# Performance work log

Measured on AMD Instinct MI355X. Metric: run time of the kernel, lower is better.

Reference implementation:

```python
import jax, jax.numpy as jnp
import numpy as np

B, S_SRC, S_TGT = 32, 128, 128
V, E, H = 32000, 256, 256
PAD_ID = 0
NEG = -1.0e9


def setup_inputs() -> dict:
    key = jax.random.key(0)
    ks = jax.random.split(key, 16)
    lengths_de = jax.random.randint(ks[0], (B,), S_SRC // 2, S_SRC + 1)
    idx_de = jax.random.randint(ks[1], (B, S_SRC), 1, V)
    pos = jnp.arange(S_SRC)[None, :]
    indices_de = jnp.where(pos < lengths_de[:, None], idx_de, PAD_ID)
    indices_en = jax.random.randint(ks[2], (B, S_TGT), 1, V)
    lengths_en = jnp.full((B,), S_TGT, dtype=jnp.int32)

    sc = 0.02
    def nrm(k, shape):
        return jax.random.normal(k, shape, dtype=jnp.float32) * sc
    emb_enc = nrm(ks[3], (V, E)).at[PAD_ID].set(0.0)
    emb_dec = nrm(ks[4], (V, E)).at[PAD_ID].set(0.0)
    return {
        "indices_de": indices_de, "lengths_de": lengths_de,
        "indices_en": indices_en, "lengths_en": lengths_en,
        "emb_enc": emb_enc, "emb_dec": emb_dec,
        "W_ih_enc": nrm(ks[5], (H, E)), "W_hh_enc": nrm(ks[6], (H, H)),
        "b_ih_enc": jnp.zeros((H,), jnp.float32), "b_hh_enc": jnp.zeros((H,), jnp.float32),
        "W_ih_dec": nrm(ks[7], (H, E)), "W_hh_dec": nrm(ks[8], (H, H)),
        "b_ih_dec": jnp.zeros((H,), jnp.float32), "b_hh_dec": jnp.zeros((H,), jnp.float32),
        "W_attn": nrm(ks[9], (H, 2 * H)), "b_attn": jnp.zeros((H,), jnp.float32),
        "W_out": nrm(ks[10], (V, H)), "b_out": jnp.zeros((V,), jnp.float32),
    }


def reference(indices_de, lengths_de, indices_en, lengths_en,
              emb_enc, emb_dec,
              W_ih_enc, W_hh_enc, b_ih_enc, b_hh_enc,
              W_ih_dec, W_hh_dec, b_ih_dec, b_hh_dec,
              W_attn, b_attn, W_out, b_out):
    # ---- Encoder: tanh RNN over packed sequence ----
    x_enc = emb_enc[indices_de]                      # [B, S, E]
    valid = jnp.arange(S_SRC)[None, :] < lengths_de[:, None]  # [B, S]

    def enc_step(h, inp):
        x_t, v_t = inp                                # [B,E], [B]
        h_new = jnp.tanh(x_t @ W_ih_enc.T + b_ih_enc + h @ W_hh_enc.T + b_hh_enc)
        h = jnp.where(v_t[:, None], h_new, h)         # frozen past length (pack semantics)
        out = jnp.where(v_t[:, None], h_new, 0.0)     # padded outputs are zero
        return h, out

    h0 = jnp.zeros((B, H), jnp.float32)
    h_final, enc_outs = jax.lax.scan(
        enc_step, h0, (x_enc.transpose(1, 0, 2), valid.T))
    encoder_outputs = enc_outs.transpose(1, 0, 2)     # [B, S, H]
    enc_mask = indices_de == PAD_ID                   # [B, S] True at padding

    # ---- Decoder: per-step RNN cell + dot-product attention + vocab proj ----
    x_dec = emb_dec[indices_en]                       # [B, T, E]

    def dec_step(h, x_t):
        h = jnp.tanh(x_t @ W_ih_dec.T + b_ih_dec + h @ W_hh_dec.T + b_hh_dec)
        scores = jnp.einsum('bh,bsh->bs', h, encoder_outputs)
        scores = jnp.where(enc_mask, NEG, scores)
        attn = jax.nn.softmax(scores, axis=-1)
        context = jnp.einsum('bs,bsh->bh', attn, encoder_outputs)
        combined = jnp.concatenate([context, h], axis=1)          # [B, 2H]
        attn_out = jnp.tanh(combined @ W_attn.T + b_attn)         # [B, H]
        logits_t = attn_out @ W_out.T + b_out                     # [B, V]
        return h, logits_t

    _, logits = jax.lax.scan(dec_step, h_final, x_dec.transpose(1, 0, 2))
    return logits.transpose(1, 0, 2)                  # [B, T, V]
```

## Files before the change

### kernel.cpp

```cpp
#include <hip/hip_runtime.h>
#include <stdint.h>

#define B_ 32
#define S_ 128
#define T_ 128
#define V_ 32000
#define E_ 256
#define H_ 256
#define NEG_ (-1.0e9f)

typedef __attribute__((ext_vector_type(8))) short short8;
typedef __attribute__((ext_vector_type(4))) float floatx4;

__device__ __forceinline__ unsigned short f2bf(float x){
  unsigned u = __float_as_uint(x);
  u = u + 0x7fffu + ((u >> 16) & 1u);
  return (unsigned short)(u >> 16);
}
__device__ __forceinline__ float bf2f(unsigned short s){
  return __uint_as_float(((unsigned)s) << 16);
}
__device__ __forceinline__ float hsum4(float4 v){ return (v.x+v.y)+(v.z+v.w); }
__device__ __forceinline__ void unpack8(uint4 q, float4& lo, float4& hi){
  lo.x = __uint_as_float(q.x << 16); lo.y = __uint_as_float(q.x & 0xffff0000u);
  lo.z = __uint_as_float(q.y << 16); lo.w = __uint_as_float(q.y & 0xffff0000u);
  hi.x = __uint_as_float(q.z << 16); hi.y = __uint_as_float(q.z & 0xffff0000u);
  hi.z = __uint_as_float(q.w << 16); hi.w = __uint_as_float(q.w & 0xffff0000u);
}

#define GLOAD_LDS16(gptr, lptr) \
  __builtin_amdgcn_global_load_lds( \
      (const __attribute__((address_space(1))) unsigned int*)(const void*)(gptr), \
      (__attribute__((address_space(3))) unsigned int*)(void*)(lptr), 16, 0, 0)

#define LDS_BARRIER() do { \
    asm volatile("s_waitcnt lgkmcnt(0)" ::: "memory"); \
    __builtin_amdgcn_s_barrier(); \
  } while(0)

__device__ __forceinline__ void cvt_body(const float* __restrict__ src,
                                         unsigned short* __restrict__ dst,
                                         int blk, int n4){
  int i = blk*256 + (int)threadIdx.x;
  if (i < n4){
    float4 v = ((const float4*)src)[i];
    ushort4 o; o.x=f2bf(v.x); o.y=f2bf(v.y); o.z=f2bf(v.z); o.w=f2bf(v.w);
    ((ushort4*)dst)[i] = o;
  }
}

__device__ __forceinline__ void xih_body(
    const int* __restrict__ idxmat, const float* __restrict__ emb,
    const float* __restrict__ Wih,
    const float* __restrict__ b1, const float* __restrict__ b2,
    float* __restrict__ out, int blk,
    int* idx_s, float4 (*x_s)[64])
{
  int b = blk >> 3;
  int t0 = (blk & 7) << 4;
  int tid = threadIdx.x;
  if (tid < 16) idx_s[tid] = idxmat[b*128 + t0 + tid];
  __syncthreads();
  for (int r = 0; r < 16; ++r)
    ((float*)&x_s[r][0])[tid] = emb[(size_t)idx_s[r]*E_ + tid];
  __syncthreads();
  int j2 = tid & 127, tg = tid >> 7;
  const float4* W0 = (const float4*)(Wih + (size_t)j2*E_);
  const float4* W1 = (const float4*)(Wih + (size_t)(j2+128)*E_);
  float4 a0[8], a1[8];
  #pragma unroll
  for (int t=0;t<8;++t){ a0[t]={0,0,0,0}; a1[t]={0,0,0,0}; }
  for (int e4 = 0; e4 < 64; ++e4){
    float4 w0 = W0[e4], w1 = W1[e4];
    #pragma unroll
    for (int t = 0; t < 8; ++t){
      float4 xv = x_s[tg*8+t][e4];
      a0[t] += w0*xv; a1[t] += w1*xv;
    }
  }
  float bi0 = b1[j2] + b2[j2];
  float bi1 = b1[j2+128] + b2[j2+128];
  #pragma unroll
  for (int t = 0; t < 8; ++t){
    size_t row = (size_t)((b<<7) + t0 + tg*8 + t)*H_;
    out[row + j2]     = hsum4(a0[t]) + bi0;
    out[row + j2+128] = hsum4(a1[t]) + bi1;
  }
}

__global__ __launch_bounds__(256) void k_prep(
    const float* __restrict__ W_out, unsigned short* __restrict__ Wout_bf,
    const float* __restrict__ W_attn, unsigned short* __restrict__ Wattn_bf,
    const int* __restrict__ indices_de, const float* __restrict__ emb_enc,
    const float* __restrict__ W_ih_enc, const float* __restrict__ b_ih_enc,
    const float* __restrict__ b_hh_enc, float* __restrict__ Xih_enc,
    const int* __restrict__ indices_en, const float* __restrict__ emb_dec,
    const float* __restrict__ W_ih_dec, const float* __restrict__ b_ih_dec,
    const float* __restrict__ b_hh_dec, float* __restrict__ Xih_dec)
{
  __shared__ int idx_s[16];
  __shared__ float4 x_s[16][64];
  int bx = blockIdx.x;
  if (bx < 8000){
    cvt_body(W_out, Wout_bf, bx, 2048000);
  } else if (bx < 8128){
    cvt_body(W_attn, Wattn_bf, bx - 8000, 32768);
  } else if (bx < 8384){
    xih_body(indices_de, emb_enc, W_ih_enc, b_ih_enc, b_hh_enc, Xih_enc,
             bx - 8128, idx_s, x_s);
  } else {
    xih_body(indices_en, emb_dec, W_ih_dec, b_ih_dec, b_hh_dec, Xih_dec,
             bx - 8384, idx_s, x_s);
  }
}

__global__ __launch_bounds__(512, 2) void k_rnn2(
    const float* __restrict__ Whh_e, const float* __restrict__ Whh_d,
    const float* __restrict__ Xih_e, const float* __restrict__ Xih_d,
    const int* __restrict__ lengths,
    unsigned short* __restrict__ enc_out,
    float* __restrict__ hseq)
{
  __shared__ float h_s[256];
  __shared__ float part[8][256];
  int b = blockIdx.x, tid = threadIdx.x;
  int kk = tid >> 6;
  int jg = tid & 63;
  float4 w[4][8];
  #pragma unroll
  for (int r = 0; r < 4; ++r){
    const float4* Wr = (const float4*)(Whh_e + (size_t)(jg + (r<<6))*H_ + (kk<<5));
    #pragma unroll
    for (int i = 0; i < 8; ++i) w[r][i] = Wr[i];
  }
  if (tid < 256) h_s[tid] = 0.f;
  int len = lengths[b];
  __syncthreads();

  for (int t = 0; t < 128; ++t){
    float x = 0.f;
    if (tid < 256) x = Xih_e[(size_t)((b<<7) + t)*H_ + tid];
    const float4* h4 = ((const float4*)h_s) + (kk << 3);
    float4 hv[8];
    #pragma unroll
    for (int i = 0; i < 8; ++i) hv[i] = h4[i];
    #pragma unroll
    for (int r = 0; r < 4; ++r){
      float4 a = {0,0,0,0};
      #pragma unroll
      for (int i = 0; i < 8; ++i) a += w[r][i]*hv[i];
      part[kk][jg + (r<<6)] = hsum4(a);
    }
    LDS_BARRIER();
    if (tid < 256){
      float s = x;
      #pragma unroll
      for (int q = 0; q < 8; ++q) s += part[q][tid];
      float hn = tanhf(s);
      float hold = h_s[tid];
      bool v = (t < len);
      h_s[tid] = v ? hn : hold;
      enc_out[(size_t)((b<<7)+t)*H_ + tid] = f2bf(v ? hn : 0.f);
    }
    LDS_BARRIER();
  }

  #pragma unroll
  for (int r = 0; r < 4; ++r){
    const float4* Wr = (const float4*)(Whh_d + (size_t)(jg + (r<<6))*H_ + (kk<<5));
    #pragma unroll
    for (int i = 0; i < 8; ++i) w[r][i] = Wr[i];
  }
  for (int t = 0; t < 128; ++t){
    float x = 0.f;
    if (tid < 256) x = Xih_d[(size_t)((b<<7) + t)*H_ + tid];
    const float4* h4 = ((const float4*)h_s) + (kk << 3);
    float4 hv[8];
    #pragma unroll
    for (int i = 0; i < 8; ++i) hv[i] = h4[i];
    #pragma unroll
    for (int r = 0; r < 4; ++r){
      float4 a = {0,0,0,0};
      #pragma unroll
      for (int i = 0; i < 8; ++i) a += w[r][i]*hv[i];
      part[kk][jg + (r<<6)] = hsum4(a);
    }
    LDS_BARRIER();
    if (tid < 256){
      float s = x;
      #pragma unroll
      for (int q = 0; q < 8; ++q) s += part[q][tid];
      float hn = tanhf(s);
      h_s[tid] = hn;
      hseq[(size_t)((b<<7)+t)*H_ + tid] = hn;
    }
    LDS_BARRIER();
  }
}

__global__ __launch_bounds__(256) void k_attn(
    const unsigned short* __restrict__ enc_out,
    const float* __restrict__ hseq,
    const int* __restrict__ lengths,
    const unsigned short* __restrict__ Wattn,
    const float* __restrict__ battn,
    unsigned short* __restrict__ attn_out)
{
  __shared__ float h_sm[16][256];
  __shared__ float sc[16][132];
  __shared__ float comb[16][512];
  int bx = blockIdx.x; int b = bx >> 3; int t0 = (bx & 7) << 4;
  int tid = threadIdx.x;
  int len = lengths[b];
  for (int r = 0; r < 16; ++r)
    h_sm[r][tid] = hseq[(size_t)((b<<7) + t0 + r)*H_ + tid];
  __syncthreads();
  {
    int s = tid & 127, tg = tid >> 7;
    float4 a[8];
    #pragma unroll
    for (int t=0;t<8;++t) a[t] = {0,0,0,0};
    const uint4* ep = (const uint4*)(enc_out + (size_t)(b*S_ + s)*H_);
    for (int oct = 0; oct < 32; ++oct){
      uint4 q = ep[oct];
      float4 elo, ehi; unpack8(q, elo, ehi);
      #pragma unroll
      for (int t = 0; t < 8; ++t){
        const float4* hp = (const float4*)&h_sm[tg*8+t][oct*8];
        a[t] += elo*hp[0] + ehi*hp[1];
      }
    }
    #pragma unroll
    for (int t = 0; t < 8; ++t)
      sc[tg*8+t][s] = (s < len) ? hsum4(a[t]) : NEG_;
  }
  __syncthreads();
  {
    int wv = tid >> 6, ln = tid & 63;
    for (int r = 0; r < 4; ++r){
      int t = r*4 + wv;
      float v0 = sc[t][ln], v1 = sc[t][ln+64];
      float m = fmaxf(v0, v1);
      #pragma unroll
      for (int off = 32; off >= 1; off >>= 1) m = fmaxf(m, __shfl_xor(m, off));
      float e0 = __expf(v0 - m), e1 = __expf(v1 - m);
      float su = e0 + e1;
      #pragma unroll
      for (int off = 32; off >= 1; off >>= 1) su += __shfl_xor(su, off);
      float inv = 1.0f / su;
      sc[t][ln] = e0*inv; sc[t][ln+64] = e1*inv;
    }
  }
  __syncthreads();
  {
    int hd = tid & 127, tg = tid >> 7;
    float c0[8], c1[8];
    #pragma unroll
    for (int t=0;t<8;++t){ c0[t]=0.f; c1[t]=0.f; }
    for (int s4 = 0; s4 < 32; ++s4){
      float ea[4], eb[4];
      #pragma unroll
      for (int i = 0; i < 4; ++i){
        const unsigned short* er = enc_out + (size_t)(b*S_ + s4*4 + i)*H_;
        ea[i] = bf2f(er[hd]); eb[i] = bf2f(er[hd+128]);
      }
      #pragma unroll
      for (int t = 0; t < 8; ++t){
        float4 av = *(const float4*)&sc[tg*8+t][s4*4];
        c0[t] += av.x*ea[0] + av.y*ea[1] + av.z*ea[2] + av.w*ea[3];
        c1[t] += av.x*eb[0] + av.y*eb[1] + av.z*eb[2] + av.w*eb[3];
      }
    }
    #pragma unroll
    for (int t = 0; t < 8; ++t){
      comb[tg*8+t][hd]     = c0[t];
      comb[tg*8+t][hd+128] = c1[t];
    }
  }
  for (int r = 0; r < 16; ++r) comb[r][256 + tid] = h_sm[r][tid];
  __syncthreads();
  {
    int j2 = tid & 127, tg = tid >> 7;
    float4 a0[8], a1[8];
    #pragma unroll
    for (int t=0;t<8;++t){ a0[t]={0,0,0,0}; a1[t]={0,0,0,0}; }
    const uint4* W0 = (const uint4*)(Wattn + (size_t)j2*512);
    const uint4* W1 = (const uint4*)(Wattn + (size_t)(j2+128)*512);
    for (int oct = 0; oct < 64; ++oct){
      float4 w0lo, w0hi, w1lo, w1hi;
      unpack8(W0[oct], w0lo, w0hi);
      unpack8(W1[oct], w1lo, w1hi);
      #pragma unroll
      for (int t = 0; t < 8; ++t){
        const float4* cp = (const float4*)&comb[tg*8+t][oct*8];
        float4 clo = cp[0], chi = cp[1];
        a0[t] += w0lo*clo + w0hi*chi;
        a1[t] += w1lo*clo + w1hi*chi;
      }
    }
    float bi0 = battn[j2], bi1 = battn[j2+128];
    #pragma unroll
    for (int t = 0; t < 8; ++t){
      size_t row = (size_t)((b<<7) + t0 + tg*8 + t)*H_;
      attn_out[row + j2]     = f2bf(tanhf(hsum4(a0[t]) + bi0));
      attn_out[row + j2+128] = f2bf(tanhf(hsum4(a1[t]) + bi1));
    }
  }
}

__global__ __launch_bounds__(512) void k_vocab(
    const unsigned short* __restrict__ A,
    const unsigned short* __restrict__ Wb,
    const float* __restrict__ bout,
    float* __restrict__ out)
{
  __shared__ alignas(16) unsigned short Asm[3][256*32];
  __shared__ alignas(16) unsigned short Bsm[3][128*32];
  int bid = blockIdx.x;
  int xcd = bid & 7, idx = bid >> 3;
  int nb = idx >> 1;
  int mb = (xcd << 1) | (idx & 1);
  int tid = threadIdx.x;
  int ln  = tid & 63;
  int wid = tid >> 6;
  int llo = ln & 15, lhi = ln >> 4;
  int wr = wid >> 1, wc = wid & 1;
  int mbase = mb*256, nbase = nb*128;

  int ca0 = tid, ca1 = tid + 512, cb = tid;
  int ra0 = ca0 >> 2, sa0 = (ca0 & 3) ^ ((ra0 >> 1) & 3);
  int ra1 = ca1 >> 2, sa1 = (ca1 & 3) ^ ((ra1 >> 1) & 3);
  int rb  = cb  >> 2, sb  = (cb  & 3) ^ ((rb  >> 1) & 3);
  const unsigned short* Ag0 = A  + (size_t)(mbase + ra0)*256 + sa0*8;
  const unsigned short* Ag1 = A  + (size_t)(mbase + ra1)*256 + sa1*8;
  const unsigned short* Bg  = Wb + (size_t)(nbase + rb )*256 + sb*8;

#define STAGE_V(bufi, kk) do { \
    GLOAD_LDS16(Ag0 + (kk), &Asm[bufi][ca0*8]); \
    GLOAD_LDS16(Ag1 + (kk), &Asm[bufi][ca1*8]); \
    GLOAD_LDS16(Bg  + (kk), &Bsm[bufi][cb*8]); \
  } while(0)

  floatx4 acc[4][4];
  #pragma unroll
  for (int mi=0;mi<4;++mi)
    #pragma unroll
    for (int ni=0;ni<4;++ni) acc[mi][ni] = (floatx4){0.f,0.f,0.f,0.f};

  int q = (llo >> 1) & 3;
  int aoff[4], boff[4];
  #pragma unroll
  for (int i=0;i<4;++i){
    aoff[i] = (wr*64 + i*16 + llo)*32 + ((lhi ^ q)*8);
    boff[i] = (wc*64 + i*16 + llo)*32 + ((lhi ^ q)*8);
  }

  STAGE_V(0, 0);
  STAGE_V(1, 32);

  #pragma unroll
  for (int k0 = 0; k0 < 8; ++k0){
    int cur = k0 % 3;
    if (k0 < 7) asm volatile("s_waitcnt vmcnt(3)" ::: "memory");
    else        asm volatile("s_waitcnt vmcnt(0)" ::: "memory");
    __builtin_amdgcn_s_barrier();

    short8 afr[4], bfr[4];
    #pragma unroll
    for (int mi=0;mi<4;++mi) afr[mi] = *(const short8*)&Asm[cur][aoff[mi]];
    #pragma unroll
    for (int ni=0;ni<4;++ni) bfr[ni] = *(const short8*)&Bsm[cur][boff[ni]];

    asm volatile("s_waitcnt lgkmcnt(0)" ::: "memory");
    __builtin_amdgcn_s_barrier();
    if (k0 < 6) STAGE_V((k0+2)%3, (k0+2)*32);

    #pragma unroll
    for (int ni=0;ni<4;++ni)
      #pragma unroll
      for (int mi=0;mi<4;++mi)
        acc[mi][ni] = __builtin_amdgcn_mfma_f32_16x16x32_bf16(afr[mi], bfr[ni], acc[mi][ni], 0, 0, 0);
  }

  #pragma unroll
  for (int ni = 0; ni < 4; ++ni){
    int col = nbase + wc*64 + ni*16 + llo;
    float bias = bout[col];
    #pragma unroll
    for (int mi = 0; mi < 4; ++mi){
      #pragma unroll
      for (int r = 0; r < 4; ++r){
        int row = mbase + wr*64 + mi*16 + lhi*4 + r;
        out[(size_t)row*V_ + col] = acc[mi][ni][r] + bias;
      }
    }
  }
#undef STAGE_V
}

extern "C" void kernel_launch(void* const* d_in, const int* in_sizes, int n_in,
                              void* d_out, int out_size, void* d_ws, size_t ws_size,
                              hipStream_t stream){
  const int*   indices_de = (const int*)d_in[0];
  const int*   lengths_de = (const int*)d_in[1];
  const int*   indices_en = (const int*)d_in[2];
  const float* emb_enc   = (const float*)d_in[4];
  const float* emb_dec   = (const float*)d_in[5];
  const float* W_ih_enc  = (const float*)d_in[6];
  const float* W_hh_enc  = (const float*)d_in[7];
  const float* b_ih_enc  = (const float*)d_in[8];
  const float* b_hh_enc  = (const float*)d_in[9];
  const float* W_ih_dec  = (const float*)d_in[10];
  const float* W_hh_dec  = (const float*)d_in[11];
  const float* b_ih_dec  = (const float*)d_in[12];
  const float* b_hh_dec  = (const float*)d_in[13];
  const float* W_attn    = (const float*)d_in[14];
  const float* b_attn    = (const float*)d_in[15];
  const float* W_out     = (const float*)d_in[16];
  const float* b_out     = (const float*)d_in[17];

  char* ws = (char*)d_ws;
  size_t o = 0;
  float* Xih_enc = (float*)(ws + o); o += (size_t)4096*256*4;
  float* Xih_dec = (float*)(ws + o); o += (size_t)4096*256*4;
  unsigned short* enc_bf = (unsigned short*)(ws + o); o += (size_t)4096*256*2;
  float* hdec    = (float*)(ws + o); o += (size_t)4096*256*4;
  unsigned short* attn_o  = (unsigned short*)(ws + o); o += (size_t)4096*256*2;
  unsigned short* Wout_bf = (unsigned short*)(ws + o); o += (size_t)V_*256*2;
  unsigned short* Wattn_bf= (unsigned short*)(ws + o); o += (size_t)256*512*2;

  k_prep<<<8640, 256, 0, stream>>>(
      W_out, Wout_bf, W_attn, Wattn_bf,
      indices_de, emb_enc, W_ih_enc, b_ih_enc, b_hh_enc, Xih_enc,
      indices_en, emb_dec, W_ih_dec, b_ih_dec, b_hh_dec, Xih_dec);
  k_rnn2<<<32, 512, 0, stream>>>(W_hh_enc, W_hh_dec, Xih_enc, Xih_dec,
                                 lengths_de, enc_bf, hdec);
  k_attn<<<256, 256, 0, stream>>>(enc_bf, hdec, lengths_de, Wattn_bf, b_attn, attn_o);
  k_vocab<<<4000, 512, 0, stream>>>(attn_o, Wout_bf, b_out, (float*)d_out);
}
```

Before: 988.4 us.

## Restructure vocab GEMM into barrier-free per-wave private LDS tiles

The vocab projection kernel changes from a 512-thread block sharing a 256x128 tile across eight waves to a 256-thread block where each wave stages its own 64x64 A/B tiles into private LDS double buffers. This removes all block-level barriers from the K loop and changes the grid mapping to 8000 blocks with a new XCD-aware block order. The trade-off is that each wave loads its own B tile, so weight traffic is duplicated across waves. Wave-private prefetch also relies on per-wave vmcnt ordering for correctness.

```diff
diff --git a/kernel.cpp b/kernel.cpp
--- a/kernel.cpp
+++ b/kernel.cpp
@@ -308,37 +308,44 @@
   }
 }
 
-__global__ __launch_bounds__(512) void k_vocab(
+__global__ __launch_bounds__(256) void k_vocab(
     const unsigned short* __restrict__ A,
     const unsigned short* __restrict__ Wb,
     const float* __restrict__ bout,
     float* __restrict__ out)
 {
-  __shared__ alignas(16) unsigned short Asm[3][256*32];
-  __shared__ alignas(16) unsigned short Bsm[3][128*32];
+  __shared__ alignas(16) unsigned short Aw[4][2][64*32];
+  __shared__ alignas(16) unsigned short Bw[4][2][64*32];
   int bid = blockIdx.x;
-  int xcd = bid & 7, idx = bid >> 3;
-  int nb = idx >> 1;
-  int mb = (xcd << 1) | (idx & 1);
+  int xcd = bid & 7;
+  int gid = xcd*1000 + (bid >> 3);
+  int mb = gid & 15, nb = gid >> 4;
   int tid = threadIdx.x;
   int ln  = tid & 63;
-  int wid = tid >> 6;
+  int w   = tid >> 6;
   int llo = ln & 15, lhi = ln >> 4;
-  int wr = wid >> 1, wc = wid & 1;
-  int mbase = mb*256, nbase = nb*128;
-
-  int ca0 = tid, ca1 = tid + 512, cb = tid;
-  int ra0 = ca0 >> 2, sa0 = (ca0 & 3) ^ ((ra0 >> 1) & 3);
-  int ra1 = ca1 >> 2, sa1 = (ca1 & 3) ^ ((ra1 >> 1) & 3);
-  int rb  = cb  >> 2, sb  = (cb  & 3) ^ ((rb  >> 1) & 3);
-  const unsigned short* Ag0 = A  + (size_t)(mbase + ra0)*256 + sa0*8;
-  const unsigned short* Ag1 = A  + (size_t)(mbase + ra1)*256 + sa1*8;
-  const unsigned short* Bg  = Wb + (size_t)(nbase + rb )*256 + sb*8;
-
-#define STAGE_V(bufi, kk) do { \
-    GLOAD_LDS16(Ag0 + (kk), &Asm[bufi][ca0*8]); \
-    GLOAD_LDS16(Ag1 + (kk), &Asm[bufi][ca1*8]); \
-    GLOAD_LDS16(Bg  + (kk), &Bsm[bufi][cb*8]); \
+  int mbase = mb*256 + w*64, nbase = nb*64;
+
+  int rowb = ln >> 2;
+  int slot = (ln & 3) ^ ((ln >> 3) & 3);
+  const unsigned short* Ag = A  + (size_t)(mbase + rowb)*256 + slot*8;
+  const unsigned short* Bg = Wb + (size_t)(nbase + rowb)*256 + slot*8;
+  unsigned short* AwB = &Aw[w][0][0];
+  unsigned short* BwB = &Bw[w][0][0];
+
+#define STAGE_T(bufi, kt) do { \
+    const unsigned short* As_ = Ag + (kt)*32; \
+    const unsigned short* Bs_ = Bg + (kt)*32; \
+    unsigned short* Ad_ = AwB + (bufi)*2048; \
+    unsigned short* Bd_ = BwB + (bufi)*2048; \
+    GLOAD_LDS16(As_ +     0, Ad_ +    0); \
+    GLOAD_LDS16(As_ +  4096, Ad_ +  512); \
+    GLOAD_LDS16(As_ +  8192, Ad_ + 1024); \
+    GLOAD_LDS16(As_ + 12288, Ad_ + 1536); \
+    GLOAD_LDS16(Bs_ +     0, Bd_ +    0); \
+    GLOAD_LDS16(Bs_ +  4096, Bd_ +  512); \
+    GLOAD_LDS16(Bs_ +  8192, Bd_ + 1024); \
+    GLOAD_LDS16(Bs_ + 12288, Bd_ + 1536); \
   } while(0)
 
   floatx4 acc[4][4];
@@ -348,33 +355,27 @@
     for (int ni=0;ni<4;++ni) acc[mi][ni] = (floatx4){0.f,0.f,0.f,0.f};
 
   int q = (llo >> 1) & 3;
-  int aoff[4], boff[4];
-  #pragma unroll
-  for (int i=0;i<4;++i){
-    aoff[i] = (wr*64 + i*16 + llo)*32 + ((lhi ^ q)*8);
-    boff[i] = (wc*64 + i*16 + llo)*32 + ((lhi ^ q)*8);
-  }
-
-  STAGE_V(0, 0);
-  STAGE_V(1, 32);
+  int aoff[4];
+  #pragma unroll
+  for (int i=0;i<4;++i) aoff[i] = (i*16 + llo)*32 + ((lhi ^ q)*8);
+
+  STAGE_T(0, 0);
+  STAGE_T(1, 1);
 
   #pragma unroll
   for (int k0 = 0; k0 < 8; ++k0){
-    int cur = k0 % 3;
-    if (k0 < 7) asm volatile("s_waitcnt vmcnt(3)" ::: "memory");
+    if (k0 < 7) asm volatile("s_waitcnt vmcnt(8)" ::: "memory");
     else        asm volatile("s_waitcnt vmcnt(0)" ::: "memory");
-    __builtin_amdgcn_s_barrier();
-
+    int buf = k0 & 1;
+    const unsigned short* Ar = AwB + buf*2048;
+    const unsigned short* Br = BwB + buf*2048;
     short8 afr[4], bfr[4];
     #pragma unroll
-    for (int mi=0;mi<4;++mi) afr[mi] = *(const short8*)&Asm[cur][aoff[mi]];
-    #pragma unroll
-    for (int ni=0;ni<4;++ni) bfr[ni] = *(const short8*)&Bsm[cur][boff[ni]];
-
+    for (int mi=0;mi<4;++mi) afr[mi] = *(const short8*)(Ar + aoff[mi]);
+    #pragma unroll
+    for (int ni=0;ni<4;++ni) bfr[ni] = *(const short8*)(Br + aoff[ni]);
     asm volatile("s_waitcnt lgkmcnt(0)" ::: "memory");
-    __builtin_amdgcn_s_barrier();
-    if (k0 < 6) STAGE_V((k0+2)%3, (k0+2)*32);
-
+    if (k0 < 6) STAGE_T(buf, k0+2);
     #pragma unroll
     for (int ni=0;ni<4;++ni)
       #pragma unroll
@@ -384,18 +385,18 @@
 
   #pragma unroll
   for (int ni = 0; ni < 4; ++ni){
-    int col = nbase + wc*64 + ni*16 + llo;
+    int col = nbase + ni*16 + llo;
     float bias = bout[col];
     #pragma unroll
     for (int mi = 0; mi < 4; ++mi){
       #pragma unroll
       for (int r = 0; r < 4; ++r){
-        int row = mbase + wr*64 + mi*16 + lhi*4 + r;
+        int row = mbase + mi*16 + lhi*4 + r;
         out[(size_t)row*V_ + col] = acc[mi][ni][r] + bias;
       }
     }
   }
-#undef STAGE_V
+#undef STAGE_T
 }
 
 extern "C" void kernel_launch(void* const* d_in, const int* in_sizes, int n_in,
@@ -436,5 +437,5 @@
   k_rnn2<<<32, 512, 0, stream>>>(W_hh_enc, W_hh_dec, Xih_enc, Xih_dec,
                                  lengths_de, enc_bf, hdec);
   k_attn<<<256, 256, 0, stream>>>(enc_bf, hdec, lengths_de, Wattn_bf, b_attn, attn_o);
-  k_vocab<<<4000, 512, 0, stream>>>(attn_o, Wout_bf, b_out, (float*)d_out);
-}
+  k_vocab<<<8000, 256, 0, stream>>>(attn_o, Wout_bf, b_out, (float*)d_out);
+}
```

Result: slower. 1.014 ms (+2.6%).

## Restructure vocab GEMM to keep A in registers and stream full-K W tiles

Applied to the files above, without the earlier changes.

The vocab projection kernel now loads each wave's 32-row slice of activations (full K=256) into registers once. It then streams four 64-column full-K tiles of W_out through double-buffered, XOR-swizzled LDS, storing each tile's output before staging the next. Each block covers 256 rows by 256 columns, and blocks are remapped per XCD, so the grid halves to 2000 blocks. This removes repeated A staging and the short K loop, and overlaps output stores with W loads. In exchange it uses more registers and hand-tuned vmcnt values that must match the issued load and store counts.

```diff
diff --git a/kernel.cpp b/kernel.cpp
--- a/kernel.cpp
+++ b/kernel.cpp
@@ -308,94 +308,94 @@
   }
 }
 
+#define VB_STAGE(bufi, s) do { \
+    _Pragma("unroll") \
+    for (int i_ = 0; i_ < 4; ++i_){ \
+      int c_ = tid + i_*512; \
+      int r_ = c_ >> 5; \
+      int sc_ = (c_ & 31) ^ (r_ & 7); \
+      GLOAD_LDS16(Wb + (size_t)(ncol0 + (s)*64 + r_)*256 + sc_*8, \
+                  &Bsm[bufi][c_*8]); \
+    } \
+  } while(0)
+
+#define VB_STEP(s, Wlit, DOSTAGE) do { \
+    asm volatile("s_waitcnt vmcnt(" Wlit ")" ::: "memory"); \
+    __builtin_amdgcn_s_barrier(); \
+    floatx4 acc[2][4]; \
+    _Pragma("unroll") \
+    for (int mi=0;mi<2;++mi) \
+      _Pragma("unroll") \
+      for (int ni=0;ni<4;++ni) acc[mi][ni]=(floatx4){0.f,0.f,0.f,0.f}; \
+    _Pragma("unroll") \
+    for (int k0=0;k0<8;++k0){ \
+      short8 bfr[4]; \
+      _Pragma("unroll") \
+      for (int ni=0;ni<4;++ni) \
+        bfr[ni] = *(const short8*)&Bsm[(s)&1][(ni*16+llo)*256 + (((k0*4+lhi)^(llo&7))<<3)]; \
+      _Pragma("unroll") \
+      for (int ni=0;ni<4;++ni){ \
+        acc[0][ni] = __builtin_amdgcn_mfma_f32_16x16x32_bf16(af[0][k0], bfr[ni], acc[0][ni], 0,0,0); \
+        acc[1][ni] = __builtin_amdgcn_mfma_f32_16x16x32_bf16(af[1][k0], bfr[ni], acc[1][ni], 0,0,0); \
+      } \
+    } \
+    asm volatile("s_waitcnt lgkmcnt(0)" ::: "memory"); \
+    __builtin_amdgcn_s_barrier(); \
+    _Pragma("unroll") \
+    for (int ni=0;ni<4;++ni){ \
+      int col_ = ncol0 + (s)*64 + ni*16 + llo; \
+      _Pragma("unroll") \
+      for (int mi=0;mi<2;++mi){ \
+        _Pragma("unroll") \
+        for (int r_=0;r_<4;++r_){ \
+          int row_ = mrow0 + mi*16 + lhi*4 + r_; \
+          out[(size_t)row_*V_ + col_] = acc[mi][ni][r_] + bpre[s][ni]; \
+        } \
+      } \
+    } \
+    asm volatile("" ::: "memory"); \
+    if (DOSTAGE) VB_STAGE((s)&1, (s)+2); \
+    asm volatile("" ::: "memory"); \
+  } while(0)
+
 __global__ __launch_bounds__(512) void k_vocab(
     const unsigned short* __restrict__ A,
     const unsigned short* __restrict__ Wb,
     const float* __restrict__ bout,
     float* __restrict__ out)
 {
-  __shared__ alignas(16) unsigned short Asm[3][256*32];
-  __shared__ alignas(16) unsigned short Bsm[3][128*32];
+  __shared__ alignas(16) unsigned short Bsm[2][64*256];
   int bid = blockIdx.x;
-  int xcd = bid & 7, idx = bid >> 3;
-  int nb = idx >> 1;
-  int mb = (xcd << 1) | (idx & 1);
+  int xcd = bid & 7;
+  int gid = xcd*250 + (bid >> 3);
+  int mb = gid / 125, ng = gid % 125;
   int tid = threadIdx.x;
   int ln  = tid & 63;
-  int wid = tid >> 6;
+  int w   = tid >> 6;
   int llo = ln & 15, lhi = ln >> 4;
-  int wr = wid >> 1, wc = wid & 1;
-  int mbase = mb*256, nbase = nb*128;
-
-  int ca0 = tid, ca1 = tid + 512, cb = tid;
-  int ra0 = ca0 >> 2, sa0 = (ca0 & 3) ^ ((ra0 >> 1) & 3);
-  int ra1 = ca1 >> 2, sa1 = (ca1 & 3) ^ ((ra1 >> 1) & 3);
-  int rb  = cb  >> 2, sb  = (cb  & 3) ^ ((rb  >> 1) & 3);
-  const unsigned short* Ag0 = A  + (size_t)(mbase + ra0)*256 + sa0*8;
-  const unsigned short* Ag1 = A  + (size_t)(mbase + ra1)*256 + sa1*8;
-  const unsigned short* Bg  = Wb + (size_t)(nbase + rb )*256 + sb*8;
-
-#define STAGE_V(bufi, kk) do { \
-    GLOAD_LDS16(Ag0 + (kk), &Asm[bufi][ca0*8]); \
-    GLOAD_LDS16(Ag1 + (kk), &Asm[bufi][ca1*8]); \
-    GLOAD_LDS16(Bg  + (kk), &Bsm[bufi][cb*8]); \
-  } while(0)
-
-  floatx4 acc[4][4];
-  #pragma unroll
-  for (int mi=0;mi<4;++mi)
-    #pragma unroll
-    for (int ni=0;ni<4;++ni) acc[mi][ni] = (floatx4){0.f,0.f,0.f,0.f};
-
-  int q = (llo >> 1) & 3;
-  int aoff[4], boff[4];
-  #pragma unroll
-  for (int i=0;i<4;++i){
-    aoff[i] = (wr*64 + i*16 + llo)*32 + ((lhi ^ q)*8);
-    boff[i] = (wc*64 + i*16 + llo)*32 + ((lhi ^ q)*8);
-  }
-
-  STAGE_V(0, 0);
-  STAGE_V(1, 32);
-
-  #pragma unroll
-  for (int k0 = 0; k0 < 8; ++k0){
-    int cur = k0 % 3;
-    if (k0 < 7) asm volatile("s_waitcnt vmcnt(3)" ::: "memory");
-    else        asm volatile("s_waitcnt vmcnt(0)" ::: "memory");
-    __builtin_amdgcn_s_barrier();
-
-    short8 afr[4], bfr[4];
-    #pragma unroll
-    for (int mi=0;mi<4;++mi) afr[mi] = *(const short8*)&Asm[cur][aoff[mi]];
-    #pragma unroll
-    for (int ni=0;ni<4;++ni) bfr[ni] = *(const short8*)&Bsm[cur][boff[ni]];
-
-    asm volatile("s_waitcnt lgkmcnt(0)" ::: "memory");
-    __builtin_amdgcn_s_barrier();
-    if (k0 < 6) STAGE_V((k0+2)%3, (k0+2)*32);
-
+  int mrow0 = mb*256 + w*32;
+  int ncol0 = ng*256;
+
+  short8 af[2][8];
+  #pragma unroll
+  for (int mi=0;mi<2;++mi)
+    #pragma unroll
+    for (int k0=0;k0<8;++k0)
+      af[mi][k0] = *(const short8*)(A + (size_t)(mrow0 + mi*16 + llo)*256 + k0*32 + lhi*8);
+  float bpre[4][4];
+  #pragma unroll
+  for (int s=0;s<4;++s)
     #pragma unroll
     for (int ni=0;ni<4;++ni)
-      #pragma unroll
-      for (int mi=0;mi<4;++mi)
-        acc[mi][ni] = __builtin_amdgcn_mfma_f32_16x16x32_bf16(afr[mi], bfr[ni], acc[mi][ni], 0, 0, 0);
-  }
-
-  #pragma unroll
-  for (int ni = 0; ni < 4; ++ni){
-    int col = nbase + wc*64 + ni*16 + llo;
-    float bias = bout[col];
-    #pragma unroll
-    for (int mi = 0; mi < 4; ++mi){
-      #pragma unroll
-      for (int r = 0; r < 4; ++r){
-        int row = mbase + wr*64 + mi*16 + lhi*4 + r;
-        out[(size_t)row*V_ + col] = acc[mi][ni][r] + bias;
-      }
-    }
-  }
-#undef STAGE_V
+      bpre[s][ni] = bout[ncol0 + s*64 + ni*16 + llo];
+
+  VB_STAGE(0, 0);
+  VB_STAGE(1, 1);
+
+  VB_STEP(0, "4",  1);
+  VB_STEP(1, "36", 1);
+  VB_STEP(2, "36", 0);
+  VB_STEP(3, "32", 0);
 }
 
 extern "C" void kernel_launch(void* const* d_in, const int* in_sizes, int n_in,
@@ -436,5 +436,5 @@
   k_rnn2<<<32, 512, 0, stream>>>(W_hh_enc, W_hh_dec, Xih_enc, Xih_dec,
                                  lengths_de, enc_bf, hdec);
   k_attn<<<256, 256, 0, stream>>>(enc_bf, hdec, lengths_de, Wattn_bf, b_attn, attn_o);
-  k_vocab<<<4000, 512, 0, stream>>>(attn_o, Wout_bf, b_out, (float*)d_out);
-}
+  k_vocab<<<2000, 512, 0, stream>>>(attn_o, Wout_bf, b_out, (float*)d_out);
+}
```

After: 943.9 us. 1.05x faster.
